# Kernel optimization log

Measured on AMD Instinct MI355X. Metric: run time of the kernel, lower is better.

## Reference

```python
import jax, jax.numpy as jnp
import numpy as np

B, N, H, E, L = 64, 100, 128, 128, 3  # batch, nodes, node_hidden, edge_hidden, gcn layers


def setup_inputs() -> dict:
    key = jax.random.key(0)
    ks = jax.random.split(key, 12)
    s = 0.05
    return dict(
        node=jax.random.normal(ks[0], (B, N, 2), jnp.float32),
        demand=jax.random.uniform(ks[1], (B, N), jnp.float32),
        dis=jax.random.uniform(ks[2], (B, N, N), jnp.float32),
        Wn0=jax.random.normal(ks[3], (3, H), jnp.float32) * s,
        bn0=jnp.zeros((H,), jnp.float32),
        Ws=jax.random.normal(ks[4], (L, H, H), jnp.float32) * s,
        Wngh=jax.random.normal(ks[5], (L, H, H), jnp.float32) * s,
        We=jax.random.normal(ks[6], (E,), jnp.float32) * s,
        be=jnp.zeros((E,), jnp.float32),
        Wih=jax.random.normal(ks[7], (2, H, 3 * H), jnp.float32) * s,
        Whh=jax.random.normal(ks[8], (2, H, 3 * H), jnp.float32) * s,
        bih=jnp.zeros((2, 3 * H), jnp.float32),
        bhh=jnp.zeros((2, 3 * H), jnp.float32),
        Wq=jax.random.normal(ks[9], (H, H), jnp.float32) * s,
        Wc=jax.random.normal(ks[10], (E, 2), jnp.float32) * s,
        bc=jnp.zeros((2,), jnp.float32),
    )


def _gru(xin, h, Wih, Whh, bih, bhh):
    gi = xin @ Wih + bih
    gh = h @ Whh + bhh
    ir, iz, inn = jnp.split(gi, 3, -1)
    hr, hz, hn = jnp.split(gh, 3, -1)
    r = jax.nn.sigmoid(ir + hr)
    z = jax.nn.sigmoid(iz + hz)
    n = jnp.tanh(inn + r * hn)
    return (1.0 - z) * n + z * h


def _decode(x, Wih, Whh, bih, bhh, Wq, sample, key):
    b, n, h = x.shape
    scale = 1.0 / np.sqrt(h).astype(np.float32)

    def step(carry, _):
        last, hid, k = carry
        emb = x[jnp.arange(b), last]                      # [b,h]
        h0 = _gru(emb, hid[0], Wih[0], Whh[0], bih[0], bhh[0])
        h1 = _gru(h0, hid[1], Wih[1], Whh[1], bih[1], bhh[1])
        logits = jnp.einsum('bh,bnh->bn', h1 @ Wq, x) * scale
        logp = jax.nn.log_softmax(logits, -1)
        k, sk = jax.random.split(k)
        if sample:
            ind = jax.random.categorical(sk, logits)
        else:
            ind = jnp.argmax(logits, -1)
        ind = ind.astype(jnp.int32)
        chosen = jnp.take_along_axis(logp, ind[:, None], 1)[:, 0]
        return (ind, jnp.stack([h0, h1]), k), (ind, chosen)

    init = (jnp.zeros((b,), jnp.int32), jnp.zeros((2, b, h), x.dtype), key)
    _, (inds, lps) = jax.lax.scan(step, init, None, length=n - 1)
    solution = jnp.concatenate([jnp.zeros((b, 1), jnp.int32), inds.T], axis=1)  # depot 0 first
    return lps.T, solution  # logprob [b,n-1], solution [b,n]


def _count_dist(sol, dis):
    bidx = jnp.arange(sol.shape[0])[:, None]
    return dis[bidx, sol[:, :-1], sol[:, 1:]].sum(axis=1, keepdims=True)  # [b,1]


def reference(node, demand, dis, Wn0, bn0, Ws, Wngh, We, be, Wih, Whh, bih, bhh, Wq, Wc, bc):
    # --- GCN encoder ---
    h = jax.nn.relu(jnp.concatenate([node, demand[..., None]], -1) @ Wn0 + bn0)  # [B,N,H]
    A = jax.nn.softmax(-dis, -1)  # distance-based soft adjacency
    for l in range(Ws.shape[0]):
        h = jax.nn.relu(h @ Ws[l] + jnp.einsum('bij,bjh->bih', A, h @ Wngh[l]))
    e = jax.nn.relu(dis[..., None] * We + be)  # [B,N,N,E]

    key = jax.random.key(42)
    k1, _ = jax.random.split(key)
    sample_logprob, sample_solution = _decode(h, Wih, Whh, bih, bhh, Wq, True, k1)
    sample_distance = _count_dist(sample_solution, dis)
    _, greedy_solution = _decode(h, Wih, Whh, bih, bhh, Wq, False, k1)
    greedy_distance = _count_dist(greedy_solution, dis)

    predict_matrix = jax.nn.softmax(e @ Wc + bc, -1)  # [B,N,N,2]

    b, n = h.shape[0], h.shape[1]
    bidx = jnp.arange(b)[:, None]
    greedy_solution_matrix = (
        jnp.zeros((b, n, n), jnp.int32)
        .at[bidx, greedy_solution[:, :-1], greedy_solution[:, 1:]]
        .set(1)
    )
    return (sample_logprob, sample_distance, greedy_distance, predict_matrix, greedy_solution_matrix)
```

## Files before the change

kernel.cpp:

```cpp
#include <hip/hip_runtime.h>
#include <math.h>

#define BB 64
#define NN 100
#define HH 128
#define T3 384

#define O0 0
#define O1 6336
#define O2 6400
#define O3 6464
#define O4 1286464

#define TINYF 1.17549435e-38f
#define SCALEF 0.08838834764831845f

__device__ __forceinline__ unsigned rotl32(unsigned x, int d) {
    return (x << d) | (x >> (32 - d));
}

__device__ __forceinline__ void tf2x32(unsigned ks0, unsigned ks1,
                                       unsigned x0, unsigned x1,
                                       unsigned& o0, unsigned& o1) {
    unsigned ks2 = ks0 ^ ks1 ^ 0x1BD11BDAu;
    x0 += ks0; x1 += ks1;
    x0 += x1; x1 = rotl32(x1, 13); x1 ^= x0;
    x0 += x1; x1 = rotl32(x1, 15); x1 ^= x0;
    x0 += x1; x1 = rotl32(x1, 26); x1 ^= x0;
    x0 += x1; x1 = rotl32(x1, 6);  x1 ^= x0;
    x0 += ks1; x1 += ks2 + 1u;
    x0 += x1; x1 = rotl32(x1, 17); x1 ^= x0;
    x0 += x1; x1 = rotl32(x1, 29); x1 ^= x0;
    x0 += x1; x1 = rotl32(x1, 16); x1 ^= x0;
    x0 += x1; x1 = rotl32(x1, 24); x1 ^= x0;
    x0 += ks2; x1 += ks0 + 2u;
    x0 += x1; x1 = rotl32(x1, 13); x1 ^= x0;
    x0 += x1; x1 = rotl32(x1, 15); x1 ^= x0;
    x0 += x1; x1 = rotl32(x1, 26); x1 ^= x0;
    x0 += x1; x1 = rotl32(x1, 6);  x1 ^= x0;
    x0 += ks0; x1 += ks1 + 3u;
    x0 += x1; x1 = rotl32(x1, 17); x1 ^= x0;
    x0 += x1; x1 = rotl32(x1, 29); x1 ^= x0;
    x0 += x1; x1 = rotl32(x1, 16); x1 ^= x0;
    x0 += x1; x1 = rotl32(x1, 24); x1 ^= x0;
    x0 += ks1; x1 += ks2 + 4u;
    x0 += x1; x1 = rotl32(x1, 13); x1 ^= x0;
    x0 += x1; x1 = rotl32(x1, 15); x1 ^= x0;
    x0 += x1; x1 = rotl32(x1, 26); x1 ^= x0;
    x0 += x1; x1 = rotl32(x1, 6);  x1 ^= x0;
    x0 += ks2; x1 += ks0 + 5u;
    o0 = x0; o1 = x1;
}

__device__ __forceinline__ float gumbel_f(unsigned k0, unsigned k1, unsigned f) {
    unsigned o0, o1;
    tf2x32(k0, k1, 0u, f, o0, o1);
    unsigned bits = o0 ^ o1;
    float u01 = __uint_as_float((bits >> 9) | 0x3F800000u) - 1.0f;
    float u = fmaxf(TINYF, u01 * (1.0f - TINYF) + TINYF);
    return -logf(-logf(u));
}


__global__ void k_embed(const float* __restrict__ node, const float* __restrict__ demand,
                        const float* __restrict__ Wn0, const float* __restrict__ bn0,
                        float* __restrict__ h) {
    int idx = blockIdx.x * 256 + threadIdx.x;
    if (idx >= BB * NN * HH) return;
    int r = idx >> 7, c = idx & 127;
    float v = node[r * 2] * Wn0[c] + node[r * 2 + 1] * Wn0[128 + c]
            + demand[r] * Wn0[256 + c] + bn0[c];
    h[idx] = fmaxf(v, 0.0f);
}

__global__ void k_adj(const float* __restrict__ dis, float* __restrict__ A) {
    int row = blockIdx.x;
    const float* d = dis + row * NN;
    int l = threadIdx.x;
    float v0 = (l < NN) ? -d[l] : -__builtin_inff();
    float v1 = (l + 64 < NN) ? -d[l + 64] : -__builtin_inff();
    float m = fmaxf(v0, v1);
    for (int off = 32; off > 0; off >>= 1) m = fmaxf(m, __shfl_xor(m, off));
    float e0 = (l < NN) ? expf(v0 - m) : 0.0f;
    float e1 = (l + 64 < NN) ? expf(v1 - m) : 0.0f;
    float s = e0 + e1;
    for (int off = 32; off > 0; off >>= 1) s += __shfl_xor(s, off);
    float inv = 1.0f / s;
    if (l < NN) A[row * NN + l] = e0 * inv;
    if (l + 64 < NN) A[row * NN + l + 64] = e1 * inv;
}

__global__ void k_hw(const float* __restrict__ h, const float* __restrict__ W,
                     float* __restrict__ out) {
    __shared__ float hs[8 * 128];
    int block_row = blockIdx.x * 8;
    int tid = threadIdx.x;
    int col = tid & 127;
    int rg = tid >> 7;
    for (int i = tid; i < 8 * 128; i += 256) hs[i] = h[block_row * 128 + i];
    __syncthreads();
    float acc[4] = {0.f, 0.f, 0.f, 0.f};
    for (int k = 0; k < 128; k++) {
        float w = W[k * 128 + col];
#pragma unroll
        for (int r = 0; r < 4; r++) acc[r] += hs[(rg + 2 * r) * 128 + k] * w;
    }
#pragma unroll
    for (int r = 0; r < 4; r++)
        out[(block_row + rg + 2 * r) * 128 + col] = acc[r];
}

__global__ void k_mm384(const float* __restrict__ h, const float* __restrict__ W,
                        const float* __restrict__ bias, float* __restrict__ out) {
    __shared__ float hs[8 * 128];
    int block_row = blockIdx.x * 8;
    int tid = threadIdx.x;
    int col = blockIdx.y * 128 + (tid & 127);
    int rg = tid >> 7;
    for (int i = tid; i < 8 * 128; i += 256) hs[i] = h[block_row * 128 + i];
    __syncthreads();
    float acc[4] = {0.f, 0.f, 0.f, 0.f};
    for (int k = 0; k < 128; k++) {
        float w = W[k * 384 + col];
#pragma unroll
        for (int r = 0; r < 4; r++) acc[r] += hs[(rg + 2 * r) * 128 + k] * w;
    }
    float b = bias[col];
#pragma unroll
    for (int r = 0; r < 4; r++)
        out[(block_row + rg + 2 * r) * 384 + col] = acc[r] + b;
}

__global__ void k_transpose128(const float* __restrict__ Wq, float* __restrict__ WqT) {
    int i = blockIdx.x * 256 + threadIdx.x;
    if (i >= 128 * 128) return;
    int k = i >> 7, c = i & 127;
    WqT[k * 128 + c] = Wq[c * 128 + k];
}

__global__ void k_agg(const float* __restrict__ h, const float* __restrict__ Ws,
                      const float* __restrict__ A, const float* __restrict__ hw,
                      float* __restrict__ out) {
    __shared__ float hs[4 * 128];
    __shared__ float As[4 * 100];
    int b = blockIdx.x / 25;
    int i0 = (blockIdx.x % 25) * 4;
    int tid = threadIdx.x;
    int col = tid & 127;
    int rg = tid >> 7;
    int rowbase = b * NN + i0;
    for (int idx = tid; idx < 4 * 128; idx += 256) hs[idx] = h[rowbase * 128 + idx];
    for (int idx = tid; idx < 4 * 100; idx += 256) As[idx] = A[rowbase * 100 + idx];
    __syncthreads();
    float acc0 = 0.f, acc1 = 0.f;
    for (int k = 0; k < 128; k++) {
        float w = Ws[k * 128 + col];
        acc0 += hs[rg * 128 + k] * w;
        acc1 += hs[(rg + 2) * 128 + k] * w;
    }
    const float* hwb = hw + b * NN * 128;
    for (int j = 0; j < NN; j++) {
        float v = hwb[j * 128 + col];
        acc0 += As[rg * 100 + j] * v;
        acc1 += As[(rg + 2) * 100 + j] * v;
    }
    out[(rowbase + rg) * 128 + col]     = fmaxf(acc0, 0.0f);
    out[(rowbase + rg + 2) * 128 + col] = fmaxf(acc1, 0.0f);
}

__global__ void k_predict(const float* __restrict__ dis, const float* __restrict__ We,
                          const float* __restrict__ be, const float* __restrict__ Wc,
                          const float* __restrict__ bc, float* __restrict__ out3) {
    __shared__ float sWe[128], sbe[128], sc0[128], sc1[128];
    int tid = threadIdx.x;
    if (tid < 128) {
        sWe[tid] = We[tid];
        sbe[tid] = be[tid];
        sc0[tid] = Wc[tid * 2];
        sc1[tid] = Wc[tid * 2 + 1];
    }
    __syncthreads();
    float b0 = bc[0], b1 = bc[1];
    for (int pos = blockIdx.x * 256 + tid; pos < BB * NN * NN; pos += gridDim.x * 256) {
        float d = dis[pos];
        float a0 = b0, a1 = b1;
        for (int k = 0; k < 128; k++) {
            float e = fmaxf(d * sWe[k] + sbe[k], 0.0f);
            a0 += e * sc0[k];
            a1 += e * sc1[k];
        }
        float m = fmaxf(a0, a1);
        float p0 = expf(a0 - m), p1 = expf(a1 - m);
        float inv = 1.0f / (p0 + p1);
        out3[pos * 2]     = p0 * inv;
        out3[pos * 2 + 1] = p1 * inv;
    }
}

__global__ void k_zero(float* __restrict__ p, int n) {
    int i = blockIdx.x * 256 + threadIdx.x;
    if (i < n) p[i] = 0.0f;
}

__device__ __forceinline__ void matvec_tile4(const float* __restrict__ W,
                                             const float* __restrict__ hp,
                                             int nk4,
                                             float* __restrict__ pg0,
                                             float* __restrict__ pg1) {
    float a00 = 0.f, a01 = 0.f, a02 = 0.f, a03 = 0.f;
    float a10 = 0.f, a11 = 0.f, a12 = 0.f, a13 = 0.f;
#pragma unroll 4
    for (int k4 = 0; k4 < nk4; ++k4) {
        float4 hA = *(const float4*)(hp + 4 * k4);
        float4 hB = *(const float4*)(hp + 132 + 4 * k4);
        const float* Wk = W + (size_t)(4 * k4) * T3;
        float4 w0 = *(const float4*)(Wk);
        float4 w1 = *(const float4*)(Wk + T3);
        float4 w2 = *(const float4*)(Wk + 2 * T3);
        float4 w3 = *(const float4*)(Wk + 3 * T3);
        a00 += hA.x * w0.x; a01 += hA.x * w0.y; a02 += hA.x * w0.z; a03 += hA.x * w0.w;
        a10 += hB.x * w0.x; a11 += hB.x * w0.y; a12 += hB.x * w0.z; a13 += hB.x * w0.w;
        a00 += hA.y * w1.x; a01 += hA.y * w1.y; a02 += hA.y * w1.z; a03 += hA.y * w1.w;
        a10 += hB.y * w1.x; a11 += hB.y * w1.y; a12 += hB.y * w1.z; a13 += hB.y * w1.w;
        a00 += hA.z * w2.x; a01 += hA.z * w2.y; a02 += hA.z * w2.z; a03 += hA.z * w2.w;
        a10 += hB.z * w2.x; a11 += hB.z * w2.y; a12 += hB.z * w2.z; a13 += hB.z * w2.w;
        a00 += hA.w * w3.x; a01 += hA.w * w3.y; a02 += hA.w * w3.z; a03 += hA.w * w3.w;
        a10 += hB.w * w3.x; a11 += hB.w * w3.y; a12 += hB.w * w3.z; a13 += hB.w * w3.w;
    }
    float4 o;
    o.x = a00; o.y = a01; o.z = a02; o.w = a03;
    *(float4*)pg0 = o;
    o.x = a10; o.y = a11; o.z = a12; o.w = a13;
    *(float4*)pg1 = o;
}

__global__ __launch_bounds__(512, 2) void k_decode4(
    const float* __restrict__ P0,
    const float* __restrict__ Z,
    const float* __restrict__ dis,
    const float* __restrict__ Wih,
    const float* __restrict__ Whh,
    const float* __restrict__ bih,
    const float* __restrict__ bhh,
    float* __restrict__ out) {
    __shared__ float Zs[NN * 132];
    __shared__ float h0s[2 * 132], h1s[2 * 132];
    __shared__ float gi0s[2 * 384];
    __shared__ float pgA[2 * 2 * 392];
    __shared__ float pgB[2 * 2 * 392];
    __shared__ float pgC[4 * 2 * 392];
    __shared__ float sbhh0[T3], sbih1[T3], sbhh1[T3];
    __shared__ float pl[2 * 2 * 100];
    __shared__ float gum[128];
    __shared__ int s_ind2[2];

    const int tid = threadIdx.x;
    const int b = blockIdx.x;

    const float* __restrict__ Wih1 = Wih + 128 * T3;

    for (int i4 = tid; i4 < NN * 32; i4 += 512) {
        int r = i4 >> 5, c4 = (i4 & 31) * 4;
        *(float4*)&Zs[r * 132 + c4] = *(const float4*)&Z[(b * NN + r) * 128 + c4];
    }
    if (tid < T3) {
        sbhh0[tid] = bhh[tid];
        sbih1[tid] = bih[T3 + tid];
        sbhh1[tid] = bhh[T3 + tid];
    }
    if (tid < 256) {
        int m = tid >> 7, i = tid & 127;
        h0s[m * 132 + i] = 0.0f;
        h1s[m * 132 + i] = 0.0f;
    }
    if (tid == 0) { s_ind2[0] = 0; s_ind2[1] = 0; }

    unsigned kk0, kk1;
    tf2x32(0u, 42u, 0u, 0u, kk0, kk1);

    int lastm = 0;
    float dist = 0.0f;
    __syncthreads();

    for (int t = 0; t < NN - 1; t++) {
        if (tid < 384) {
            const int unit = tid / 192;
            const int r = tid - unit * 192;
            const int ks = r / 96, j4 = r - ks * 96;
            const int j0 = j4 * 4, k0 = ks * 64;
            const float* W = Whh + unit * (128 * T3) + (size_t)k0 * T3 + j0;
            const float* hp = ((unit == 0) ? h0s : h1s) + k0;
            float* pg = (unit == 0) ? pgA : pgB;
            matvec_tile4(W, hp, 16,
                         &pg[(ks * 2 + 0) * 392 + j0],
                         &pg[(ks * 2 + 1) * 392 + j0]);
        } else {
            int u = tid - 384;
            int l0 = s_ind2[0], l1 = s_ind2[1];
#pragma unroll
            for (int q = 0; q < 6; q++) {
                int f = u + 128 * q;
                int m = (f >= 384) ? 1 : 0;
                int j = f - m * 384;
                gi0s[f] = P0[(size_t)(b * NN + (m ? l1 : l0)) * T3 + j];
            }
            unsigned sk0, sk1, nk0, nk1;
            tf2x32(kk0, kk1, 0u, 1u, sk0, sk1);
            tf2x32(kk0, kk1, 0u, 0u, nk0, nk1);
            kk0 = nk0; kk1 = nk1;
            if (u < NN) gum[u] = gumbel_f(sk0, sk1, (unsigned)(b * NN + u));
        }
        __syncthreads();

        if (tid < 256) {
            int m = tid >> 7, i = tid & 127;
            float ghr = pgA[(0 * 2 + m) * 392 + i]       + pgA[(1 * 2 + m) * 392 + i]       + sbhh0[i];
            float ghz = pgA[(0 * 2 + m) * 392 + i + 128] + pgA[(1 * 2 + m) * 392 + i + 128] + sbhh0[i + 128];
            float ghn = pgA[(0 * 2 + m) * 392 + i + 256] + pgA[(1 * 2 + m) * 392 + i + 256] + sbhh0[i + 256];
            float rr = 1.0f / (1.0f + expf(-(gi0s[m * 384 + i] + ghr)));
            float zz = 1.0f / (1.0f + expf(-(gi0s[m * 384 + i + 128] + ghz)));
            float nn = tanhf(gi0s[m * 384 + i + 256] + rr * ghn);
            h0s[m * 132 + i] = (1.0f - zz) * nn + zz * h0s[m * 132 + i];
        }
        __syncthreads();

        if (tid < 384) {
            const int ks = tid / 96, j4 = tid - ks * 96;
            const int j0 = j4 * 4, k0 = ks * 32;
            const float* W = Wih1 + (size_t)k0 * T3 + j0;
            matvec_tile4(W, h0s + k0, 8,
                         &pgC[(ks * 2 + 0) * 392 + j0],
                         &pgC[(ks * 2 + 1) * 392 + j0]);
        }
        __syncthreads();

        if (tid < 256) {
            int m = tid >> 7, i = tid & 127;
            float gir = sbih1[i], giz = sbih1[i + 128], gin = sbih1[i + 256];
#pragma unroll
            for (int ks = 0; ks < 4; ks++) {
                int pb = (ks * 2 + m) * 392;
                gir += pgC[pb + i];
                giz += pgC[pb + i + 128];
                gin += pgC[pb + i + 256];
            }
            float ghr = pgB[(0 * 2 + m) * 392 + i]       + pgB[(1 * 2 + m) * 392 + i]       + sbhh1[i];
            float ghz = pgB[(0 * 2 + m) * 392 + i + 128] + pgB[(1 * 2 + m) * 392 + i + 128] + sbhh1[i + 128];
            float ghn = pgB[(0 * 2 + m) * 392 + i + 256] + pgB[(1 * 2 + m) * 392 + i + 256] + sbhh1[i + 256];
            float rr = 1.0f / (1.0f + expf(-(gir + ghr)));
            float zz = 1.0f / (1.0f + expf(-(giz + ghz)));
            float nn = tanhf(gin + rr * ghn);
            h1s[m * 132 + i] = (1.0f - zz) * nn + zz * h1s[m * 132 + i];
        }
        __syncthreads();

        if (tid < 200) {
            int ks = tid / 100, n = tid - ks * 100;
            int k0 = ks * 64;
            const float* Zp = &Zs[n * 132 + k0];
            const float* hp = &h1s[k0];
            float a0 = 0.f, a1 = 0.f;
#pragma unroll 4
            for (int q = 0; q < 16; q++) {
                float4 z4 = *(const float4*)(Zp + 4 * q);
                float4 hA = *(const float4*)(hp + 4 * q);
                float4 hB = *(const float4*)(hp + 132 + 4 * q);
                a0 += hA.x * z4.x; a0 += hA.y * z4.y; a0 += hA.z * z4.z; a0 += hA.w * z4.w;
                a1 += hB.x * z4.x; a1 += hB.y * z4.y; a1 += hB.z * z4.z; a1 += hB.w * z4.w;
            }
            pl[(0 * 2 + ks) * 100 + n] = a0;
            pl[(1 * 2 + ks) * 100 + n] = a1;
        }
        __syncthreads();

        if (tid < 128) {
            const int m = tid >> 6, lane = tid & 63;
            float v0, v1 = -__builtin_inff();
            v0 = (pl[(m * 2 + 0) * 100 + lane] + pl[(m * 2 + 1) * 100 + lane]) * SCALEF;
            if (lane + 64 < NN)
                v1 = (pl[(m * 2 + 0) * 100 + lane + 64] + pl[(m * 2 + 1) * 100 + lane + 64]) * SCALEF;
            float mx = fmaxf(v0, v1);
            for (int off = 32; off > 0; off >>= 1) mx = fmaxf(mx, __shfl_xor(mx, off));
            float e = expf(v0 - mx) + ((lane + 64 < NN) ? expf(v1 - mx) : 0.0f);
            for (int off = 32; off > 0; off >>= 1) e += __shfl_xor(e, off);
            float a0 = v0, a1 = v1;
            if (m == 0) {
                a0 += gum[lane];
                if (lane + 64 < NN) a1 += gum[lane + 64];
            }
            float bv; int bi;
            if (a1 > a0) { bv = a1; bi = lane + 64; } else { bv = a0; bi = lane; }
            for (int off = 32; off > 0; off >>= 1) {
                float ov = __shfl_xor(bv, off);
                int   oi = __shfl_xor(bi, off);
                if (ov > bv || (ov == bv && oi < bi)) { bv = ov; bi = oi; }
            }
            int ind = bi;
            float la = __shfl(v0, ind & 63);
            float lb = __shfl(v1, ind & 63);
            float lv = (ind < 64) ? la : lb;
            if (lane == 0) {
                if (m == 0) out[O0 + b * (NN - 1) + t] = lv - mx - logf(e);
                else        out[O4 + (size_t)b * NN * NN + lastm * NN + ind] = 1.0f;
                s_ind2[m] = ind;
            }
            dist += dis[b * NN * NN + lastm * NN + ind];
            lastm = ind;
        }
        __syncthreads();
    }

    if (tid == 0)  out[O1 + b] = dist;
    if (tid == 64) out[O2 + b] = dist;
}

__global__ __launch_bounds__(768) void k_decode2(
    const float* __restrict__ P0, const float* __restrict__ Z,
    const float* __restrict__ dis,
    const float* __restrict__ Wih, const float* __restrict__ Whh,
    const float* __restrict__ bih, const float* __restrict__ bhh,
    float* __restrict__ out) {
    __shared__ float Zs[NN * 129];
    __shared__ float h0s[128], h1s[128];
    __shared__ float gi0s[T3];
    __shared__ float pg0[2 * T3];
    __shared__ float gi1s[T3], gh1s[T3];
    __shared__ float sbhh0[T3], sbih1[T3], sbhh1[T3];
    __shared__ float plx[4 * NN];
    __shared__ float logits[NN];
    __shared__ float s_m, s_s;
    __shared__ int s_ind;

    const int tid = threadIdx.x;
    const int b = blockIdx.x >> 1;
    const int greedy = blockIdx.x & 1;

    const float* Whh0 = Whh;
    const float* Wih1 = Wih + 128 * T3;
    const float* Whh1 = Whh + 128 * T3;

    for (int idx = tid; idx < NN * 128; idx += 768) {
        int r = idx >> 7, c = idx & 127;
        Zs[r * 129 + c] = Z[(b * NN + r) * 128 + c];
    }
    if (tid < T3) {
        sbhh0[tid] = bhh[tid];
        sbih1[tid] = bih[T3 + tid];
        sbhh1[tid] = bhh[T3 + tid];
    }
    if (tid < 128) { h0s[tid] = 0.0f; h1s[tid] = 0.0f; }

    unsigned kk0, kk1;
    tf2x32(0u, 42u, 0u, 0u, kk0, kk1);

    int last = 0;
    float dist = 0.0f;
    __syncthreads();

    for (int t = 0; t < NN - 1; t++) {
        unsigned sk0, sk1, nk0, nk1;
        tf2x32(kk0, kk1, 0u, 1u, sk0, sk1);
        tf2x32(kk0, kk1, 0u, 0u, nk0, nk1);
        kk0 = nk0; kk1 = nk1;

        {
            const float* P0row = P0 + (size_t)(b * NN + last) * T3;
            if (tid < T3) {
                int j = tid;
                float acc = 0.0f;
                for (int k = 0; k < 64; k++) acc += h0s[k] * Whh0[k * T3 + j];
                pg0[j] = acc;
                gi0s[j] = P0row[j];
            } else {
                int j = tid - T3;
                float acc = 0.0f;
                for (int k = 64; k < 128; k++) acc += h0s[k] * Whh0[k * T3 + j];
                pg0[T3 + j] = acc;
            }
        }
        __syncthreads();
        if (tid < 128) {
            float ghr = pg0[tid] + pg0[T3 + tid] + sbhh0[tid];
            float ghz = pg0[tid + 128] + pg0[T3 + tid + 128] + sbhh0[tid + 128];
            float ghn = pg0[tid + 256] + pg0[T3 + tid + 256] + sbhh0[tid + 256];
            float r = 1.0f / (1.0f + expf(-(gi0s[tid] + ghr)));
            float z = 1.0f / (1.0f + expf(-(gi0s[tid + 128] + ghz)));
            float n = tanhf(gi0s[tid + 256] + r * ghn);
            h0s[tid] = (1.0f - z) * n + z * h0s[tid];
        }
        __syncthreads();
        if (tid < T3) {
            int j = tid;
            float acc = sbih1[j];
            for (int k = 0; k < 128; k++) acc += h0s[k] * Wih1[k * T3 + j];
            gi1s[j] = acc;
        } else {
            int j = tid - T3;
            float acc = sbhh1[j];
            for (int k = 0; k < 128; k++) acc += h1s[k] * Whh1[k * T3 + j];
            gh1s[j] = acc;
        }
        __syncthreads();
        if (tid < 128) {
            float r = 1.0f / (1.0f + expf(-(gi1s[tid] + gh1s[tid])));
            float z = 1.0f / (1.0f + expf(-(gi1s[tid + 128] + gh1s[tid + 128])));
            float n = tanhf(gi1s[tid + 256] + r * gh1s[tid + 256]);
            h1s[tid] = (1.0f - z) * n + z * h1s[tid];
        }
        __syncthreads();
        if (tid < 400) {
            int n = tid % 100, p = tid / 100;
            int k0 = p * 32;
            float acc = 0.0f;
            for (int kk = 0; kk < 32; kk++) acc += h1s[k0 + kk] * Zs[n * 129 + k0 + kk];
            plx[p * 100 + n] = acc;
        }
        __syncthreads();
        if (tid < 64) {
            float v0 = -__builtin_inff(), v1 = -__builtin_inff();
            {
                int n = tid;
                v0 = (plx[n] + plx[100 + n] + plx[200 + n] + plx[300 + n]) * SCALEF;
                logits[n] = v0;
            }
            if (tid + 64 < NN) {
                int n = tid + 64;
                v1 = (plx[n] + plx[100 + n] + plx[200 + n] + plx[300 + n]) * SCALEF;
                logits[n] = v1;
            }
            float m = fmaxf(v0, v1);
            for (int off = 32; off > 0; off >>= 1) m = fmaxf(m, __shfl_xor(m, off));
            float e = expf(v0 - m) + ((tid + 64 < NN) ? expf(v1 - m) : 0.0f);
            for (int off = 32; off > 0; off >>= 1) e += __shfl_xor(e, off);
            float a0 = v0, a1 = v1;
            if (!greedy) {
                a0 = v0 + gumbel_f(sk0, sk1, (unsigned)(b * NN + tid));
                if (tid + 64 < NN) a1 = v1 + gumbel_f(sk0, sk1, (unsigned)(b * NN + tid + 64));
            }
            float bv; int bi;
            if (a1 > a0) { bv = a1; bi = tid + 64; } else { bv = a0; bi = tid; }
            for (int off = 32; off > 0; off >>= 1) {
                float ov = __shfl_xor(bv, off);
                int   oi = __shfl_xor(bi, off);
                if (ov > bv || (ov == bv && oi < bi)) { bv = ov; bi = oi; }
            }
            if (tid == 0) { s_m = m; s_s = e; s_ind = bi; }
        }
        __syncthreads();
        int ind = s_ind;
        if (tid == 0) {
            if (!greedy) out[O0 + b * (NN - 1) + t] = logits[ind] - s_m - logf(s_s);
            dist += dis[b * NN * NN + last * NN + ind];
            if (greedy) out[O4 + b * NN * NN + last * NN + ind] = 1.0f;
        }
        last = ind;
        __syncthreads();
    }
    if (tid == 0) {
        if (!greedy) out[O1 + b] = dist;
        else         out[O2 + b] = dist;
    }
}

extern "C" void kernel_launch(void* const* d_in, const int* in_sizes, int n_in,
                              void* d_out, int out_size, void* d_ws, size_t ws_size,
                              hipStream_t stream) {
    (void)in_sizes; (void)n_in; (void)out_size;
    const float* node   = (const float*)d_in[0];
    const float* demand = (const float*)d_in[1];
    const float* dis    = (const float*)d_in[2];
    const float* Wn0    = (const float*)d_in[3];
    const float* bn0    = (const float*)d_in[4];
    const float* Ws     = (const float*)d_in[5];
    const float* Wngh   = (const float*)d_in[6];
    const float* We     = (const float*)d_in[7];
    const float* be     = (const float*)d_in[8];
    const float* Wih    = (const float*)d_in[9];
    const float* Whh    = (const float*)d_in[10];
    const float* bih    = (const float*)d_in[11];
    const float* bhh    = (const float*)d_in[12];
    const float* Wq     = (const float*)d_in[13];
    const float* Wc     = (const float*)d_in[14];
    const float* bc     = (const float*)d_in[15];
    float* out = (float*)d_out;
    float* ws  = (float*)d_ws;

    float* hA  = ws;
    float* hB  = ws + 819200;
    float* hw  = ws + 1638400;
    float* A   = ws + 2457600;
    float* P0  = ws + 2457600;
    float* WqT = ws + 4915200;
    const size_t need_bytes = (size_t)4931584 * 4;
    const bool big_ws = ws_size >= need_bytes;

    hipLaunchKernelGGL(k_embed, dim3(3200), dim3(256), 0, stream, node, demand, Wn0, bn0, hA);
    hipLaunchKernelGGL(k_adj, dim3(6400), dim3(64), 0, stream, dis, A);

    float* cur = hA;
    float* nxt = hB;
    for (int l = 0; l < 3; l++) {
        hipLaunchKernelGGL(k_hw, dim3(800), dim3(256), 0, stream, cur, Wngh + l * 16384, hw);
        hipLaunchKernelGGL(k_agg, dim3(1600), dim3(256), 0, stream, cur, Ws + l * 16384, A, hw, nxt);
        float* tswap = cur; cur = nxt; nxt = tswap;
    }

    hipLaunchKernelGGL(k_predict, dim3(2500), dim3(256), 0, stream, dis, We, be, Wc, bc, out + O3);
    hipLaunchKernelGGL(k_zero, dim3(2500), dim3(256), 0, stream, out + O4, BB * NN * NN);

    hipLaunchKernelGGL(k_transpose128, dim3(64), dim3(256), 0, stream, Wq, WqT);
    hipLaunchKernelGGL(k_hw, dim3(800), dim3(256), 0, stream, cur, WqT, hw);
    hipLaunchKernelGGL(k_mm384, dim3(800, 3), dim3(256), 0, stream, cur, Wih, bih, P0);
    if (big_ws) {
        hipLaunchKernelGGL(k_decode4, dim3(64), dim3(512), 0, stream,
                           P0, hw, dis, Wih, Whh, bih, bhh, out);
    } else {
        hipLaunchKernelGGL(k_decode2, dim3(128), dim3(768), 0, stream,
                           P0, hw, dis, Wih, Whh, bih, bhh, out);
    }
}
```

Before: 979.8 us.

## Fuse setup kernels, enlarge GEMM row tiles, drop fallback decoder

Merges the embed and adjacency kernels into one launch, the predict and output-zeroing kernels into one, and the Z and P0 projections into a single 2D-grid kernel, which cuts the launch count. The GCN matmul kernels now compute 16 rows (k_hw16) or 10 rows (k_agg10) per block instead of 8 or 4, so each weight load is reused across more rows, and k_predict processes two positions per thread. The small-workspace k_decode2 fallback is removed, so the code now assumes the workspace is always large enough. Most time likely sits in the serial decode kernel, which is unchanged, so the gains are limited to the smaller preprocessing kernels.

```diff
diff --git a/kernel.cpp b/kernel.cpp
--- a/kernel.cpp
+++ b/kernel.cpp
@@ -61,74 +61,88 @@
     return -logf(-logf(u));
 }
 
-
-__global__ void k_embed(const float* __restrict__ node, const float* __restrict__ demand,
-                        const float* __restrict__ Wn0, const float* __restrict__ bn0,
-                        float* __restrict__ h) {
-    int idx = blockIdx.x * 256 + threadIdx.x;
-    if (idx >= BB * NN * HH) return;
-    int r = idx >> 7, c = idx & 127;
-    float v = node[r * 2] * Wn0[c] + node[r * 2 + 1] * Wn0[128 + c]
-            + demand[r] * Wn0[256 + c] + bn0[c];
-    h[idx] = fmaxf(v, 0.0f);
-}
-
-__global__ void k_adj(const float* __restrict__ dis, float* __restrict__ A) {
-    int row = blockIdx.x;
-    const float* d = dis + row * NN;
-    int l = threadIdx.x;
-    float v0 = (l < NN) ? -d[l] : -__builtin_inff();
-    float v1 = (l + 64 < NN) ? -d[l + 64] : -__builtin_inff();
-    float m = fmaxf(v0, v1);
-    for (int off = 32; off > 0; off >>= 1) m = fmaxf(m, __shfl_xor(m, off));
-    float e0 = (l < NN) ? expf(v0 - m) : 0.0f;
-    float e1 = (l + 64 < NN) ? expf(v1 - m) : 0.0f;
-    float s = e0 + e1;
-    for (int off = 32; off > 0; off >>= 1) s += __shfl_xor(s, off);
-    float inv = 1.0f / s;
-    if (l < NN) A[row * NN + l] = e0 * inv;
-    if (l + 64 < NN) A[row * NN + l + 64] = e1 * inv;
-}
-
-__global__ void k_hw(const float* __restrict__ h, const float* __restrict__ W,
-                     float* __restrict__ out) {
-    __shared__ float hs[8 * 128];
-    int block_row = blockIdx.x * 8;
+__global__ void k_embed_adj(const float* __restrict__ node, const float* __restrict__ demand,
+                            const float* __restrict__ Wn0, const float* __restrict__ bn0,
+                            const float* __restrict__ dis,
+                            float* __restrict__ h, float* __restrict__ A) {
+    int bid = blockIdx.x, tid = threadIdx.x;
+    if (bid < 3200) {
+        int idx = bid * 256 + tid;
+        int r = idx >> 7, c = idx & 127;
+        float v = node[r * 2] * Wn0[c] + node[r * 2 + 1] * Wn0[128 + c]
+                + demand[r] * Wn0[256 + c] + bn0[c];
+        h[idx] = fmaxf(v, 0.0f);
+    } else {
+        int row = (bid - 3200) * 4 + (tid >> 6);
+        int l = tid & 63;
+        const float* d = dis + row * NN;
+        float v0 = -d[l];
+        float v1 = (l + 64 < NN) ? -d[l + 64] : -__builtin_inff();
+        float m = fmaxf(v0, v1);
+        for (int off = 32; off > 0; off >>= 1) m = fmaxf(m, __shfl_xor(m, off));
+        float e0 = expf(v0 - m);
+        float e1 = (l + 64 < NN) ? expf(v1 - m) : 0.0f;
+        float s = e0 + e1;
+        for (int off = 32; off > 0; off >>= 1) s += __shfl_xor(s, off);
+        float inv = 1.0f / s;
+        A[row * NN + l] = e0 * inv;
+        if (l + 64 < NN) A[row * NN + l + 64] = e1 * inv;
+    }
+}
+
+__global__ void k_hw16(const float* __restrict__ h, const float* __restrict__ W,
+                       float* __restrict__ out) {
+    __shared__ float hs[16 * 128];
+    int block_row = blockIdx.x * 16;
     int tid = threadIdx.x;
     int col = tid & 127;
     int rg = tid >> 7;
-    for (int i = tid; i < 8 * 128; i += 256) hs[i] = h[block_row * 128 + i];
+    for (int i = tid; i < 16 * 128; i += 256) hs[i] = h[block_row * 128 + i];
     __syncthreads();
-    float acc[4] = {0.f, 0.f, 0.f, 0.f};
+    float acc[8] = {0.f, 0.f, 0.f, 0.f, 0.f, 0.f, 0.f, 0.f};
     for (int k = 0; k < 128; k++) {
         float w = W[k * 128 + col];
 #pragma unroll
-        for (int r = 0; r < 4; r++) acc[r] += hs[(rg + 2 * r) * 128 + k] * w;
-    }
-#pragma unroll
-    for (int r = 0; r < 4; r++)
+        for (int r = 0; r < 8; r++) acc[r] += hs[(rg + 2 * r) * 128 + k] * w;
+    }
+#pragma unroll
+    for (int r = 0; r < 8; r++)
         out[(block_row + rg + 2 * r) * 128 + col] = acc[r];
 }
 
-__global__ void k_mm384(const float* __restrict__ h, const float* __restrict__ W,
-                        const float* __restrict__ bias, float* __restrict__ out) {
-    __shared__ float hs[8 * 128];
-    int block_row = blockIdx.x * 8;
+__global__ void k_zp(const float* __restrict__ h, const float* __restrict__ WqT,
+                     const float* __restrict__ Wih, const float* __restrict__ bih,
+                     float* __restrict__ Z, float* __restrict__ P0) {
+    __shared__ float hs[16 * 128];
+    int block_row = blockIdx.x * 16;
     int tid = threadIdx.x;
-    int col = blockIdx.y * 128 + (tid & 127);
+    int c = tid & 127;
     int rg = tid >> 7;
-    for (int i = tid; i < 8 * 128; i += 256) hs[i] = h[block_row * 128 + i];
+    int y = blockIdx.y;
+    for (int i = tid; i < 16 * 128; i += 256) hs[i] = h[block_row * 128 + i];
     __syncthreads();
-    float acc[4] = {0.f, 0.f, 0.f, 0.f};
-    for (int k = 0; k < 128; k++) {
-        float w = W[k * 384 + col];
-#pragma unroll
-        for (int r = 0; r < 4; r++) acc[r] += hs[(rg + 2 * r) * 128 + k] * w;
-    }
-    float b = bias[col];
-#pragma unroll
-    for (int r = 0; r < 4; r++)
-        out[(block_row + rg + 2 * r) * 384 + col] = acc[r] + b;
+    float acc[8] = {0.f, 0.f, 0.f, 0.f, 0.f, 0.f, 0.f, 0.f};
+    if (y == 0) {
+        for (int k = 0; k < 128; k++) {
+            float w = WqT[k * 128 + c];
+#pragma unroll
+            for (int r = 0; r < 8; r++) acc[r] += hs[(rg + 2 * r) * 128 + k] * w;
+        }
+#pragma unroll
+        for (int r = 0; r < 8; r++)
+            Z[(block_row + rg + 2 * r) * 128 + c] = acc[r];
+    } else {
+        int col = (y - 1) * 128 + c;
+        for (int k = 0; k < 128; k++) {
+            float w = Wih[k * 384 + col];
+#pragma unroll
+            for (int r = 0; r < 8; r++) acc[r] += hs[(rg + 2 * r) * 128 + k] * w;
+        }
+        float bb = bih[col];
+#pragma unroll
+        for (int r = 0; r < 8; r++)
+            P0[(size_t)(block_row + rg + 2 * r) * 384 + col] = acc[r] + bb;
+    }
 }
 
 __global__ void k_transpose128(const float* __restrict__ Wq, float* __restrict__ WqT) {
@@ -138,41 +152,49 @@
     WqT[k * 128 + c] = Wq[c * 128 + k];
 }
 
-__global__ void k_agg(const float* __restrict__ h, const float* __restrict__ Ws,
-                      const float* __restrict__ A, const float* __restrict__ hw,
-                      float* __restrict__ out) {
-    __shared__ float hs[4 * 128];
-    __shared__ float As[4 * 100];
-    int b = blockIdx.x / 25;
-    int i0 = (blockIdx.x % 25) * 4;
+__global__ void k_agg10(const float* __restrict__ h, const float* __restrict__ Ws,
+                        const float* __restrict__ A, const float* __restrict__ hw,
+                        float* __restrict__ out) {
+    __shared__ float hs[10 * 128];
+    __shared__ float As[10 * 100];
+    int b = blockIdx.x / 10;
+    int i0 = (blockIdx.x % 10) * 10;
     int tid = threadIdx.x;
     int col = tid & 127;
     int rg = tid >> 7;
     int rowbase = b * NN + i0;
-    for (int idx = tid; idx < 4 * 128; idx += 256) hs[idx] = h[rowbase * 128 + idx];
-    for (int idx = tid; idx < 4 * 100; idx += 256) As[idx] = A[rowbase * 100 + idx];
+    for (int i = tid; i < 10 * 128; i += 256) hs[i] = h[rowbase * 128 + i];
+    for (int i = tid; i < 10 * 100; i += 256) As[i] = A[rowbase * 100 + i];
     __syncthreads();
-    float acc0 = 0.f, acc1 = 0.f;
+    float acc[5] = {0.f, 0.f, 0.f, 0.f, 0.f};
     for (int k = 0; k < 128; k++) {
         float w = Ws[k * 128 + col];
-        acc0 += hs[rg * 128 + k] * w;
-        acc1 += hs[(rg + 2) * 128 + k] * w;
+#pragma unroll
+        for (int r = 0; r < 5; r++) acc[r] += hs[(rg + 2 * r) * 128 + k] * w;
     }
     const float* hwb = hw + b * NN * 128;
     for (int j = 0; j < NN; j++) {
         float v = hwb[j * 128 + col];
-        acc0 += As[rg * 100 + j] * v;
-        acc1 += As[(rg + 2) * 100 + j] * v;
-    }
-    out[(rowbase + rg) * 128 + col]     = fmaxf(acc0, 0.0f);
-    out[(rowbase + rg + 2) * 128 + col] = fmaxf(acc1, 0.0f);
-}
-
-__global__ void k_predict(const float* __restrict__ dis, const float* __restrict__ We,
-                          const float* __restrict__ be, const float* __restrict__ Wc,
-                          const float* __restrict__ bc, float* __restrict__ out3) {
+#pragma unroll
+        for (int r = 0; r < 5; r++) acc[r] += As[(rg + 2 * r) * 100 + j] * v;
+    }
+#pragma unroll
+    for (int r = 0; r < 5; r++)
+        out[(rowbase + rg + 2 * r) * 128 + col] = fmaxf(acc[r], 0.0f);
+}
+
+__global__ void k_predict_zero(const float* __restrict__ dis, const float* __restrict__ We,
+                               const float* __restrict__ be, const float* __restrict__ Wc,
+                               const float* __restrict__ bc, float* __restrict__ out3,
+                               float* __restrict__ zp) {
+    int bid = blockIdx.x, tid = threadIdx.x;
+    if (bid >= 1250) {
+        int i = (bid - 1250) * 256 + tid;
+        float4 z; z.x = 0.f; z.y = 0.f; z.z = 0.f; z.w = 0.f;
+        ((float4*)zp)[i] = z;
+        return;
+    }
     __shared__ float sWe[128], sbe[128], sc0[128], sc1[128];
-    int tid = threadIdx.x;
     if (tid < 128) {
         sWe[tid] = We[tid];
         sbe[tid] = be[tid];
@@ -181,25 +203,30 @@
     }
     __syncthreads();
     float b0 = bc[0], b1 = bc[1];
-    for (int pos = blockIdx.x * 256 + tid; pos < BB * NN * NN; pos += gridDim.x * 256) {
-        float d = dis[pos];
-        float a0 = b0, a1 = b1;
-        for (int k = 0; k < 128; k++) {
-            float e = fmaxf(d * sWe[k] + sbe[k], 0.0f);
-            a0 += e * sc0[k];
-            a1 += e * sc1[k];
-        }
-        float m = fmaxf(a0, a1);
-        float p0 = expf(a0 - m), p1 = expf(a1 - m);
-        float inv = 1.0f / (p0 + p1);
-        out3[pos * 2]     = p0 * inv;
-        out3[pos * 2 + 1] = p1 * inv;
-    }
-}
-
-__global__ void k_zero(float* __restrict__ p, int n) {
-    int i = blockIdx.x * 256 + threadIdx.x;
-    if (i < n) p[i] = 0.0f;
+    int p0 = bid * 512 + tid, p1 = p0 + 256;
+    float d0 = dis[p0], d1 = dis[p1];
+    float a00 = b0, a01 = b1, a10 = b0, a11 = b1;
+    for (int k = 0; k < 128; k++) {
+        float we = sWe[k], bbe = sbe[k], c0 = sc0[k], c1 = sc1[k];
+        float e0 = fmaxf(d0 * we + bbe, 0.0f);
+        float e1 = fmaxf(d1 * we + bbe, 0.0f);
+        a00 += e0 * c0; a01 += e0 * c1;
+        a10 += e1 * c0; a11 += e1 * c1;
+    }
+    {
+        float m = fmaxf(a00, a01);
+        float q0 = expf(a00 - m), q1 = expf(a01 - m);
+        float inv = 1.0f / (q0 + q1);
+        out3[p0 * 2] = q0 * inv;
+        out3[p0 * 2 + 1] = q1 * inv;
+    }
+    {
+        float m = fmaxf(a10, a11);
+        float q0 = expf(a10 - m), q1 = expf(a11 - m);
+        float inv = 1.0f / (q0 + q1);
+        out3[p1 * 2] = q0 * inv;
+        out3[p1 * 2 + 1] = q1 * inv;
+    }
 }
 
 __device__ __forceinline__ void matvec_tile4(const float* __restrict__ W,
@@ -235,13 +262,10 @@
 }
 
 __global__ __launch_bounds__(512, 2) void k_decode4(
-    const float* __restrict__ P0,
-    const float* __restrict__ Z,
+    const float* __restrict__ P0, const float* __restrict__ Z,
     const float* __restrict__ dis,
-    const float* __restrict__ Wih,
-    const float* __restrict__ Whh,
-    const float* __restrict__ bih,
-    const float* __restrict__ bhh,
+    const float* __restrict__ Wih, const float* __restrict__ Whh,
+    const float* __restrict__ bih, const float* __restrict__ bhh,
     float* __restrict__ out) {
     __shared__ float Zs[NN * 132];
     __shared__ float h0s[2 * 132], h1s[2 * 132];
@@ -256,7 +280,6 @@
 
     const int tid = threadIdx.x;
     const int b = blockIdx.x;
-
     const float* __restrict__ Wih1 = Wih + 128 * T3;
 
     for (int i4 = tid; i4 < NN * 32; i4 += 512) {
@@ -356,9 +379,9 @@
 
         if (tid < 200) {
             int ks = tid / 100, n = tid - ks * 100;
-            int k0 = ks * 64;
-            const float* Zp = &Zs[n * 132 + k0];
-            const float* hp = &h1s[k0];
+            int kk0p = ks * 64;
+            const float* Zp = &Zs[n * 132 + kk0p];
+            const float* hp = &h1s[kk0p];
             float a0 = 0.f, a1 = 0.f;
 #pragma unroll 4
             for (int q = 0; q < 16; q++) {
@@ -414,158 +437,10 @@
     if (tid == 64) out[O2 + b] = dist;
 }
 
-__global__ __launch_bounds__(768) void k_decode2(
-    const float* __restrict__ P0, const float* __restrict__ Z,
-    const float* __restrict__ dis,
-    const float* __restrict__ Wih, const float* __restrict__ Whh,
-    const float* __restrict__ bih, const float* __restrict__ bhh,
-    float* __restrict__ out) {
-    __shared__ float Zs[NN * 129];
-    __shared__ float h0s[128], h1s[128];
-    __shared__ float gi0s[T3];
-    __shared__ float pg0[2 * T3];
-    __shared__ float gi1s[T3], gh1s[T3];
-    __shared__ float sbhh0[T3], sbih1[T3], sbhh1[T3];
-    __shared__ float plx[4 * NN];
-    __shared__ float logits[NN];
-    __shared__ float s_m, s_s;
-    __shared__ int s_ind;
-
-    const int tid = threadIdx.x;
-    const int b = blockIdx.x >> 1;
-    const int greedy = blockIdx.x & 1;
-
-    const float* Whh0 = Whh;
-    const float* Wih1 = Wih + 128 * T3;
-    const float* Whh1 = Whh + 128 * T3;
-
-    for (int idx = tid; idx < NN * 128; idx += 768) {
-        int r = idx >> 7, c = idx & 127;
-        Zs[r * 129 + c] = Z[(b * NN + r) * 128 + c];
-    }
-    if (tid < T3) {
-        sbhh0[tid] = bhh[tid];
-        sbih1[tid] = bih[T3 + tid];
-        sbhh1[tid] = bhh[T3 + tid];
-    }
-    if (tid < 128) { h0s[tid] = 0.0f; h1s[tid] = 0.0f; }
-
-    unsigned kk0, kk1;
-    tf2x32(0u, 42u, 0u, 0u, kk0, kk1);
-
-    int last = 0;
-    float dist = 0.0f;
-    __syncthreads();
-
-    for (int t = 0; t < NN - 1; t++) {
-        unsigned sk0, sk1, nk0, nk1;
-        tf2x32(kk0, kk1, 0u, 1u, sk0, sk1);
-        tf2x32(kk0, kk1, 0u, 0u, nk0, nk1);
-        kk0 = nk0; kk1 = nk1;
-
-        {
-            const float* P0row = P0 + (size_t)(b * NN + last) * T3;
-            if (tid < T3) {
-                int j = tid;
-                float acc = 0.0f;
-                for (int k = 0; k < 64; k++) acc += h0s[k] * Whh0[k * T3 + j];
-                pg0[j] = acc;
-                gi0s[j] = P0row[j];
-            } else {
-                int j = tid - T3;
-                float acc = 0.0f;
-                for (int k = 64; k < 128; k++) acc += h0s[k] * Whh0[k * T3 + j];
-                pg0[T3 + j] = acc;
-            }
-        }
-        __syncthreads();
-        if (tid < 128) {
-            float ghr = pg0[tid] + pg0[T3 + tid] + sbhh0[tid];
-            float ghz = pg0[tid + 128] + pg0[T3 + tid + 128] + sbhh0[tid + 128];
-            float ghn = pg0[tid + 256] + pg0[T3 + tid + 256] + sbhh0[tid + 256];
-            float r = 1.0f / (1.0f + expf(-(gi0s[tid] + ghr)));
-            float z = 1.0f / (1.0f + expf(-(gi0s[tid + 128] + ghz)));
-            float n = tanhf(gi0s[tid + 256] + r * ghn);
-            h0s[tid] = (1.0f - z) * n + z * h0s[tid];
-        }
-        __syncthreads();
-        if (tid < T3) {
-            int j = tid;
-            float acc = sbih1[j];
-            for (int k = 0; k < 128; k++) acc += h0s[k] * Wih1[k * T3 + j];
-            gi1s[j] = acc;
-        } else {
-            int j = tid - T3;
-            float acc = sbhh1[j];
-            for (int k = 0; k < 128; k++) acc += h1s[k] * Whh1[k * T3 + j];
-            gh1s[j] = acc;
-        }
-        __syncthreads();
-        if (tid < 128) {
-            float r = 1.0f / (1.0f + expf(-(gi1s[tid] + gh1s[tid])));
-            float z = 1.0f / (1.0f + expf(-(gi1s[tid + 128] + gh1s[tid + 128])));
-            float n = tanhf(gi1s[tid + 256] + r * gh1s[tid + 256]);
-            h1s[tid] = (1.0f - z) * n + z * h1s[tid];
-        }
-        __syncthreads();
-        if (tid < 400) {
-            int n = tid % 100, p = tid / 100;
-            int k0 = p * 32;
-            float acc = 0.0f;
-            for (int kk = 0; kk < 32; kk++) acc += h1s[k0 + kk] * Zs[n * 129 + k0 + kk];
-            plx[p * 100 + n] = acc;
-        }
-        __syncthreads();
-        if (tid < 64) {
-            float v0 = -__builtin_inff(), v1 = -__builtin_inff();
-            {
-                int n = tid;
-                v0 = (plx[n] + plx[100 + n] + plx[200 + n] + plx[300 + n]) * SCALEF;
-                logits[n] = v0;
-            }
-            if (tid + 64 < NN) {
-                int n = tid + 64;
-                v1 = (plx[n] + plx[100 + n] + plx[200 + n] + plx[300 + n]) * SCALEF;
-                logits[n] = v1;
-            }
-            float m = fmaxf(v0, v1);
-            for (int off = 32; off > 0; off >>= 1) m = fmaxf(m, __shfl_xor(m, off));
-            float e = expf(v0 - m) + ((tid + 64 < NN) ? expf(v1 - m) : 0.0f);
-            for (int off = 32; off > 0; off >>= 1) e += __shfl_xor(e, off);
-            float a0 = v0, a1 = v1;
-            if (!greedy) {
-                a0 = v0 + gumbel_f(sk0, sk1, (unsigned)(b * NN + tid));
-                if (tid + 64 < NN) a1 = v1 + gumbel_f(sk0, sk1, (unsigned)(b * NN + tid + 64));
-            }
-            float bv; int bi;
-            if (a1 > a0) { bv = a1; bi = tid + 64; } else { bv = a0; bi = tid; }
-            for (int off = 32; off > 0; off >>= 1) {
-                float ov = __shfl_xor(bv, off);
-                int   oi = __shfl_xor(bi, off);
-                if (ov > bv || (ov == bv && oi < bi)) { bv = ov; bi = oi; }
-            }
-            if (tid == 0) { s_m = m; s_s = e; s_ind = bi; }
-        }
-        __syncthreads();
-        int ind = s_ind;
-        if (tid == 0) {
-            if (!greedy) out[O0 + b * (NN - 1) + t] = logits[ind] - s_m - logf(s_s);
-            dist += dis[b * NN * NN + last * NN + ind];
-            if (greedy) out[O4 + b * NN * NN + last * NN + ind] = 1.0f;
-        }
-        last = ind;
-        __syncthreads();
-    }
-    if (tid == 0) {
-        if (!greedy) out[O1 + b] = dist;
-        else         out[O2 + b] = dist;
-    }
-}
-
 extern "C" void kernel_launch(void* const* d_in, const int* in_sizes, int n_in,
                               void* d_out, int out_size, void* d_ws, size_t ws_size,
                               hipStream_t stream) {
-    (void)in_sizes; (void)n_in; (void)out_size;
+    (void)in_sizes; (void)n_in; (void)out_size; (void)ws_size;
     const float* node   = (const float*)d_in[0];
     const float* demand = (const float*)d_in[1];
     const float* dis    = (const float*)d_in[2];
@@ -591,31 +466,24 @@
     float* A   = ws + 2457600;
     float* P0  = ws + 2457600;
     float* WqT = ws + 4915200;
-    const size_t need_bytes = (size_t)4931584 * 4;
-    const bool big_ws = ws_size >= need_bytes;
-
-    hipLaunchKernelGGL(k_embed, dim3(3200), dim3(256), 0, stream, node, demand, Wn0, bn0, hA);
-    hipLaunchKernelGGL(k_adj, dim3(6400), dim3(64), 0, stream, dis, A);
+
+    hipLaunchKernelGGL(k_predict_zero, dim3(1875), dim3(256), 0, stream,
+                       dis, We, be, Wc, bc, out + O3, out + O4);
+
+    hipLaunchKernelGGL(k_embed_adj, dim3(4800), dim3(256), 0, stream,
+                       node, demand, Wn0, bn0, dis, hA, A);
 
     float* cur = hA;
     float* nxt = hB;
     for (int l = 0; l < 3; l++) {
-        hipLaunchKernelGGL(k_hw, dim3(800), dim3(256), 0, stream, cur, Wngh + l * 16384, hw);
-        hipLaunchKernelGGL(k_agg, dim3(1600), dim3(256), 0, stream, cur, Ws + l * 16384, A, hw, nxt);
+        hipLaunchKernelGGL(k_hw16, dim3(400), dim3(256), 0, stream, cur, Wngh + l * 16384, hw);
+        hipLaunchKernelGGL(k_agg10, dim3(640), dim3(256), 0, stream, cur, Ws + l * 16384, A, hw, nxt);
         float* tswap = cur; cur = nxt; nxt = tswap;
     }
 
-    hipLaunchKernelGGL(k_predict, dim3(2500), dim3(256), 0, stream, dis, We, be, Wc, bc, out + O3);
-    hipLaunchKernelGGL(k_zero, dim3(2500), dim3(256), 0, stream, out + O4, BB * NN * NN);
-
     hipLaunchKernelGGL(k_transpose128, dim3(64), dim3(256), 0, stream, Wq, WqT);
-    hipLaunchKernelGGL(k_hw, dim3(800), dim3(256), 0, stream, cur, WqT, hw);
-    hipLaunchKernelGGL(k_mm384, dim3(800, 3), dim3(256), 0, stream, cur, Wih, bih, P0);
-    if (big_ws) {
-        hipLaunchKernelGGL(k_decode4, dim3(64), dim3(512), 0, stream,
-                           P0, hw, dis, Wih, Whh, bih, bhh, out);
-    } else {
-        hipLaunchKernelGGL(k_decode2, dim3(128), dim3(768), 0, stream,
-                           P0, hw, dis, Wih, Whh, bih, bhh, out);
-    }
-}
+    hipLaunchKernelGGL(k_zp, dim3(400, 4), dim3(256), 0, stream, cur, WqT, Wih, bih, hw, P0);
+
+    hipLaunchKernelGGL(k_decode4, dim3(64), dim3(512), 0, stream,
+                       P0, hw, dis, Wih, Whh, bih, bhh, out);
+}
```

Result: no change. 979.6 us (-0.0%).
